# Optimization experiments

Hardware: AMD Instinct MI355X
Metric: run time of the kernel (lower is better)

## Reference

```python
import jax, jax.numpy as jnp
import numpy as np

N = 100000          # nodes
E = 1600000         # edges (nnz of A)
D_IN = 128
D_OUT = 128


def setup_inputs() -> dict:
    key = jax.random.key(0)
    ks = jax.random.split(key, 9)
    s = 1.0 / np.sqrt(D_IN)
    inp = {
        "h_n": jax.random.normal(ks[0], (N, D_IN), dtype=jnp.float32),
        "W_w": jax.random.uniform(ks[1], (D_OUT, D_IN), jnp.float32, -s, s),
        "W_b": jax.random.uniform(ks[2], (D_OUT,), jnp.float32, -s, s),
        "Wt_w": jax.random.uniform(ks[3], (D_OUT, D_IN), jnp.float32, -s, s),
        "Wt_b": jax.random.uniform(ks[4], (D_OUT,), jnp.float32, -s, s),
        "Ws_w": jax.random.uniform(ks[5], (D_OUT, D_IN), jnp.float32, -s, s),
        "Ws_b": jax.random.uniform(ks[6], (D_OUT,), jnp.float32, -s, s),
        # COO indices of sparse adjacency A (binary values): A[rows[e], cols[e]] = 1
        "rows": jax.random.randint(ks[7], (E,), 0, N, dtype=jnp.int64)
                if jax.config.jax_enable_x64 else
                jax.random.randint(ks[7], (E,), 0, N, dtype=jnp.int32),
        "cols": jax.random.randint(ks[8], (E,), 0, N, dtype=jnp.int32),
    }
    inp["rows"] = inp["rows"].astype(jnp.int32)
    return inp


def reference(h_n, W_w, W_b, Wt_w, Wt_b, Ws_w, Ws_b, rows, cols):
    # Dense projections: [N, D_OUT]
    Wh  = h_n @ W_w.T + W_b    # W(h_n)
    Wth = h_n @ Wt_w.T + Wt_b  # W_trans(h_n)
    Wsh = h_n @ Ws_w.T + Ws_b  # W_self(h_n)

    # A @ Wh  : out[i] = sum over edges (i=rows[e], j=cols[e]) of Wh[j]
    agg   = jax.ops.segment_sum(Wh[cols],  rows, num_segments=N)
    # A_T @ Wth : out[i] = sum over edges (j=rows[e], i=cols[e]) of Wth[j]
    agg_t = jax.ops.segment_sum(Wth[rows], cols, num_segments=N)

    # exact (erf-based) GELU, matching torch F.gelu default
    return jax.nn.gelu(agg + agg_t + Wsh, approximate=False)
```

## Files before the change

### kernel.cpp

```cpp
#include <hip/hip_runtime.h>


typedef __bf16 bf16;
typedef __bf16 bf16x4 __attribute__((ext_vector_type(4)));
typedef __bf16 bf16x8 __attribute__((ext_vector_type(8)));
typedef float  f32x4  __attribute__((ext_vector_type(4)));
typedef unsigned int u32;
typedef u32 u32x4 __attribute__((ext_vector_type(4)));
typedef unsigned short u16;

#define D 128
#define CAPC 2432
#define SLAB 2816
#define BIN_CHUNK 6400
#define EPT 25

__global__ __launch_bounds__(256) void k_bin(
    const int* __restrict__ rows, const int* __restrict__ cols,
    int* __restrict__ gcnt_f, int* __restrict__ gcnt_r,
    u32* __restrict__ buf_f, u32* __restrict__ buf_r, int E, int B,
    const float* __restrict__ h,
    const float* __restrict__ Ws_w, const float* __restrict__ W_w,
    const float* __restrict__ Wt_w,
    bf16* __restrict__ h_bf, bf16* __restrict__ wbf, int n4h) {
    __shared__ int hist[1024];
    __shared__ int lbase[1024];
    __shared__ int gbase[1024];
    __shared__ int tsum[256];
    __shared__ u32 sorted[BIN_CHUNK];
    __shared__ u16 btag[BIN_CHUNK];
    int t = threadIdx.x;

    if (blockIdx.y == 2) {
        int stride = gridDim.x * 256;
        int ncast = n4h + 32 + 12288;
        for (int i = blockIdx.x * 256 + t; i < ncast; i += stride) {
            if (i < n4h) {
                f32x4 v = *(const f32x4*)&h[i * 4];
                bf16x4 o;
                o.x = (bf16)v.x; o.y = (bf16)v.y; o.z = (bf16)v.z; o.w = (bf16)v.w;
                *(bf16x4*)&h_bf[i * 4] = o;
            } else if (i < n4h + 32) {
                int k = i - n4h;
                bf16x4 z; z.x = (bf16)0.f; z.y = (bf16)0.f; z.z = (bf16)0.f; z.w = (bf16)0.f;
                *(bf16x4*)&h_bf[(size_t)n4h * 4 + k * 4] = z;
            } else {
                int k = i - n4h - 32;
                const float* src = (k < 4096) ? Ws_w : (k < 8192) ? W_w : Wt_w;
                int kk = k & 4095;
                f32x4 v = *(const f32x4*)&src[kk * 4];
                bf16x4 o;
                o.x = (bf16)v.x; o.y = (bf16)v.y; o.z = (bf16)v.z; o.w = (bf16)v.w;
                *(bf16x4*)&wbf[k * 4] = o;
            }
        }
        return;
    }

    int dir = blockIdx.y;
    const int* key = dir ? cols : rows;
    const int* pay = dir ? rows : cols;
    int* gcnt = dir ? gcnt_r : gcnt_f;
    u32* buf  = dir ? buf_r : buf_f;
    int base = blockIdx.x * BIN_CHUNK;

    for (int b = t; b < 1024; b += 256) hist[b] = 0;
    __syncthreads();
    int kv[EPT], pv[EPT];
#pragma unroll
    for (int i = 0; i < EPT; ++i) {
        int e = base + i * 256 + t;
        if (e < E) {
            kv[i] = key[e]; pv[i] = pay[e];
            atomicAdd(&hist[kv[i] >> 7], 1);
        }
    }
    __syncthreads();
    int s0 = hist[t * 4], s1 = hist[t * 4 + 1], s2 = hist[t * 4 + 2], s3 = hist[t * 4 + 3];
    tsum[t] = s0 + s1 + s2 + s3;
    __syncthreads();
    for (int o = 1; o < 256; o <<= 1) {
        int v = (t >= o) ? tsum[t - o] : 0;
        __syncthreads();
        tsum[t] += v;
        __syncthreads();
    }
    int run = (t > 0) ? tsum[t - 1] : 0;
    lbase[t * 4]     = run;
    lbase[t * 4 + 1] = run + s0;
    lbase[t * 4 + 2] = run + s0 + s1;
    lbase[t * 4 + 3] = run + s0 + s1 + s2;
    __syncthreads();
    int total = tsum[255];
    for (int b = t; b < 1024; b += 256) {
        int nxt = (b < 1023) ? lbase[b + 1] : total;
        int c = nxt - lbase[b];
        gbase[b] = (c && b < B) ? atomicAdd(&gcnt[b], c) : 0;
        hist[b] = lbase[b];
    }
    __syncthreads();
#pragma unroll
    for (int i = 0; i < EPT; ++i) {
        int e = base + i * 256 + t;
        if (e < E) {
            int k = kv[i], p = pv[i];
            int b = k >> 7;
            int pos = atomicAdd(&hist[b], 1);
            sorted[pos] = ((u32)(k & 127) << 17) | (u32)p;
            btag[pos] = (u16)b;
        }
    }
    __syncthreads();
    for (int i = t; i < total; i += 256) {
        int b = btag[i];
        int gp = gbase[b] + (i - lbase[b]);
        if (gp < CAPC) buf[(size_t)b * SLAB + gp] = sorted[i];
    }
}

__device__ __forceinline__ float blo(u32 w) { return __uint_as_float(w << 16); }
__device__ __forceinline__ float bhi(u32 w) { return __uint_as_float(w & 0xffff0000u); }

__global__ __launch_bounds__(256) void k_aggsort(
    const u32* __restrict__ h32,
    const int* __restrict__ gcnt_f, const int* __restrict__ gcnt_r,
    const u32* __restrict__ buf_f, const u32* __restrict__ buf_r,
    bf16* __restrict__ AH, bf16* __restrict__ ATH,
    int* __restrict__ deg_f, int* __restrict__ deg_r, int N, u32 PADV) {
    __shared__ u32 sorted[SLAB];
    __shared__ int hist[128], pscn[128], cursor[128];
    int t = threadIdx.x, bkt = blockIdx.x;
    const int* cp; const u32* buf; bf16* dst; int* deg;
    if (blockIdx.y == 0) { cp = gcnt_f; buf = buf_f + (size_t)bkt * SLAB; dst = AH;  deg = deg_f; }
    else                 { cp = gcnt_r; buf = buf_r + (size_t)bkt * SLAB; dst = ATH; deg = deg_r; }
    int cnt = cp[bkt]; if (cnt > CAPC) cnt = CAPC;
    if (t < 128) hist[t] = 0;
    __syncthreads();
    for (int i = t; i < cnt; i += 256)
        atomicAdd(&hist[buf[i] >> 17], 1);
    __syncthreads();
    int pd = 0;
    if (t < 128) { pd = (hist[t] + 3) & ~3; pscn[t] = pd; }
    __syncthreads();
    for (int o = 1; o < 128; o <<= 1) {
        int v = (t < 128 && t >= o) ? pscn[t - o] : 0;
        __syncthreads();
        if (t < 128) pscn[t] += v;
        __syncthreads();
    }
    int ptot = pscn[127];
    if (t < 128) cursor[t] = pscn[t] - pd;
    __syncthreads();
    for (int i = t; i < ptot; i += 256) sorted[i] = PADV;
    __syncthreads();
    for (int i = t; i < cnt; i += 256) {
        u32 w = buf[i];
        int p = atomicAdd(&cursor[w >> 17], 1);
        sorted[p] = (w & 0x1FFFF) << 6;
    }
    __syncthreads();

    int wave = t >> 6, lane = t & 63;
    int q = lane >> 4, c = lane & 15;
    int node0 = bkt * 128;
    for (int ln = wave; ln < 128; ln += 4) {
        int node = node0 + ln;
        if (node >= N) continue;
        int dg = hist[ln];
        int plen = (dg + 3) & ~3;
        int p = pscn[ln] - plen, pend = pscn[ln];
        float a0 = 0.f, a1 = 0.f, a2 = 0.f, a3 = 0.f;
        float a4 = 0.f, a5 = 0.f, a6 = 0.f, a7 = 0.f;
        for (; p + 15 < pend; p += 16) {
            u32 j0 = sorted[p + q],     j1 = sorted[p + 4 + q];
            u32 j2 = sorted[p + 8 + q], j3 = sorted[p + 12 + q];
            u32x4 w0 = *(const u32x4*)&h32[(size_t)j0 + c * 4];
            u32x4 w1 = *(const u32x4*)&h32[(size_t)j1 + c * 4];
            u32x4 w2 = *(const u32x4*)&h32[(size_t)j2 + c * 4];
            u32x4 w3 = *(const u32x4*)&h32[(size_t)j3 + c * 4];
            a0 += blo(w0.x); a1 += bhi(w0.x); a2 += blo(w0.y); a3 += bhi(w0.y);
            a4 += blo(w0.z); a5 += bhi(w0.z); a6 += blo(w0.w); a7 += bhi(w0.w);
            a0 += blo(w1.x); a1 += bhi(w1.x); a2 += blo(w1.y); a3 += bhi(w1.y);
            a4 += blo(w1.z); a5 += bhi(w1.z); a6 += blo(w1.w); a7 += bhi(w1.w);
            a0 += blo(w2.x); a1 += bhi(w2.x); a2 += blo(w2.y); a3 += bhi(w2.y);
            a4 += blo(w2.z); a5 += bhi(w2.z); a6 += blo(w2.w); a7 += bhi(w2.w);
            a0 += blo(w3.x); a1 += bhi(w3.x); a2 += blo(w3.y); a3 += bhi(w3.y);
            a4 += blo(w3.z); a5 += bhi(w3.z); a6 += blo(w3.w); a7 += bhi(w3.w);
        }
        for (; p + 3 < pend; p += 4) {
            u32 j = sorted[p + q];
            u32x4 w = *(const u32x4*)&h32[(size_t)j + c * 4];
            a0 += blo(w.x); a1 += bhi(w.x); a2 += blo(w.y); a3 += bhi(w.y);
            a4 += blo(w.z); a5 += bhi(w.z); a6 += blo(w.w); a7 += bhi(w.w);
        }
        a0 += __shfl_down(a0, 16); a1 += __shfl_down(a1, 16);
        a2 += __shfl_down(a2, 16); a3 += __shfl_down(a3, 16);
        a4 += __shfl_down(a4, 16); a5 += __shfl_down(a5, 16);
        a6 += __shfl_down(a6, 16); a7 += __shfl_down(a7, 16);
        a0 += __shfl_down(a0, 32); a1 += __shfl_down(a1, 32);
        a2 += __shfl_down(a2, 32); a3 += __shfl_down(a3, 32);
        a4 += __shfl_down(a4, 32); a5 += __shfl_down(a5, 32);
        a6 += __shfl_down(a6, 32); a7 += __shfl_down(a7, 32);
        if (lane < 16) {
            bf16x8 o;
            o[0] = (bf16)a0; o[1] = (bf16)a1; o[2] = (bf16)a2; o[3] = (bf16)a3;
            o[4] = (bf16)a4; o[5] = (bf16)a5; o[6] = (bf16)a6; o[7] = (bf16)a7;
            *(bf16x8*)&dst[(size_t)node * D + c * 8] = o;
        }
    }
    if (t < 128) {
        int node = node0 + t;
        if (node < N) deg[node] = hist[t];
    }
}

__global__ __launch_bounds__(256) void k_gemm(
    const bf16* __restrict__ h, const bf16* __restrict__ AH, const bf16* __restrict__ ATH,
    const bf16* __restrict__ wbf,
    const float* __restrict__ Ws_b, const float* __restrict__ W_b, const float* __restrict__ Wt_b,
    const int* __restrict__ deg_out, const int* __restrict__ deg_in,
    float* __restrict__ out, int N) {
    __shared__ __align__(16) bf16 Ash[128 * 32];
    __shared__ __align__(16) bf16 Bsh[128 * 32];
    int t = threadIdx.x;
    int lane = t & 63;
    int w = t >> 6;
    int wm = (w >> 1) * 64, wn = (w & 1) * 64;
    int m0 = blockIdx.x * 128;

    f32x4 acc[4][4];
#pragma unroll
    for (int i = 0; i < 4; ++i)
#pragma unroll
        for (int j = 0; j < 4; ++j)
            acc[i][j] = (f32x4){0.f, 0.f, 0.f, 0.f};

    for (int kc = 0; kc < 12; ++kc) {
        const bf16* X  = (kc < 4) ? h : (kc < 8) ? AH : ATH;
        const bf16* Wm = wbf + (kc >> 2) * (128 * 128);
        int c0 = (kc & 3) * 32;
#pragma unroll
        for (int r = 0; r < 2; ++r) {
            int v = r * 256 + t;
            int row = v >> 2, seg = v & 3;
            int xr = m0 + row; if (xr >= N) xr = N - 1;
            *(bf16x8*)&Ash[row * 32 + seg * 8] =
                *(const bf16x8*)&X[(size_t)xr * D + c0 + seg * 8];
            *(bf16x8*)&Bsh[row * 32 + seg * 8] =
                *(const bf16x8*)&Wm[row * D + c0 + seg * 8];
        }
        __syncthreads();
        int kg = lane >> 4, lr = lane & 15;
        bf16x8 a[4], b[4];
#pragma unroll
        for (int i = 0; i < 4; ++i) {
            a[i] = *(const bf16x8*)&Ash[(wm + i * 16 + lr) * 32 + kg * 8];
            b[i] = *(const bf16x8*)&Bsh[(wn + i * 16 + lr) * 32 + kg * 8];
        }
#pragma unroll
        for (int i = 0; i < 4; ++i)
#pragma unroll
            for (int j = 0; j < 4; ++j)
                acc[i][j] = __builtin_amdgcn_mfma_f32_16x16x32_bf16(
                    a[i], b[j], acc[i][j], 0, 0, 0);
        __syncthreads();
    }

    int lr = lane & 15, lq = lane >> 4;
#pragma unroll
    for (int i = 0; i < 4; ++i) {
#pragma unroll
        for (int r = 0; r < 4; ++r) {
            int node = m0 + wm + i * 16 + lq * 4 + r;
            if (node >= N) continue;
            float fdr = (float)deg_out[node], fdc = (float)deg_in[node];
#pragma unroll
            for (int j = 0; j < 4; ++j) {
                int f = wn + j * 16 + lr;
                float val = acc[i][j][r] + Ws_b[f] + fdr * W_b[f] + fdc * Wt_b[f];
                float g = 0.5f * val * (1.0f + erff(val * 0.70710678118654752f));
                out[(size_t)node * D + f] = g;
            }
        }
    }
}

extern "C" void kernel_launch(void* const* d_in, const int* in_sizes, int n_in,
                              void* d_out, int out_size, void* d_ws, size_t ws_size,
                              hipStream_t stream) {
    const float* h    = (const float*)d_in[0];
    const float* W_w  = (const float*)d_in[1];
    const float* W_b  = (const float*)d_in[2];
    const float* Wt_w = (const float*)d_in[3];
    const float* Wt_b = (const float*)d_in[4];
    const float* Ws_w = (const float*)d_in[5];
    const float* Ws_b = (const float*)d_in[6];
    const int*   rows = (const int*)d_in[7];
    const int*   cols = (const int*)d_in[8];
    float* out = (float*)d_out;

    const int N = in_sizes[0] / D;
    const int E = in_sizes[7];
    const int B = (N + 127) >> 7;

    char* ws = (char*)d_ws;
    size_t off = 0;
    auto take = [&](size_t bytes) -> char* {
        char* p = ws + off;
        off += (bytes + 511) & ~(size_t)511;
        return p;
    };
    bf16* h_bf    = (bf16*)take((size_t)(N + 1) * D * sizeof(bf16));
    bf16* AH      = (bf16*)take((size_t)N * D * sizeof(bf16));
    bf16* ATH     = (bf16*)take((size_t)N * D * sizeof(bf16));
    bf16* wbf     = (bf16*)take((size_t)3 * 128 * 128 * sizeof(bf16));
    int*  gcnt    = (int*)take((size_t)2 * B * sizeof(int));
    int*  deg_f   = (int*)take((size_t)N * sizeof(int));
    int*  deg_r   = (int*)take((size_t)N * sizeof(int));
    u32*  buf_f   = (u32*)take((size_t)B * SLAB * sizeof(u32));
    u32*  buf_r   = (u32*)take((size_t)B * SLAB * sizeof(u32));
    int*  gcnt_f = gcnt, *gcnt_r = gcnt + B;

    hipMemsetAsync(gcnt, 0, (size_t)2 * B * sizeof(int), stream);

    int n4h = N * D / 4;
    dim3 gbin((E + BIN_CHUNK - 1) / BIN_CHUNK, 3);
    k_bin<<<gbin, 256, 0, stream>>>(rows, cols, gcnt_f, gcnt_r, buf_f, buf_r,
                                    E, B, h, Ws_w, W_w, Wt_w, h_bf, wbf, n4h);
    dim3 gagg(B, 2);
    k_aggsort<<<gagg, 256, 0, stream>>>((const u32*)h_bf, gcnt_f, gcnt_r,
                                        buf_f, buf_r, AH, ATH,
                                        deg_f, deg_r, N, (u32)N << 6);
    k_gemm<<<B, 256, 0, stream>>>(h_bf, AH, ATH, wbf,
                                  Ws_b, W_b, Wt_b,
                                  deg_f, deg_r, out, N);
}
```

Before: 319.7 us.

## Scatter binned edges directly to global slabs, dropping LDS local sort

The binning kernel no longer sorts each chunk's edges in shared memory before writing them out. It now reserves global slab ranges per bucket straight from the histogram, then writes each edge directly using a shared atomic cursor. The per-block chunk is halved, which frees a large amount of LDS and should raise occupancy while removing a scan and a copy pass. The cost is that global writes become scattered instead of contiguous per bucket, which may hurt write coalescing, and more blocks issue global atomics.

```diff
diff --git a/kernel.cpp b/kernel.cpp
--- a/kernel.cpp
+++ b/kernel.cpp
@@ -7,13 +7,12 @@
 typedef float  f32x4  __attribute__((ext_vector_type(4)));
 typedef unsigned int u32;
 typedef u32 u32x4 __attribute__((ext_vector_type(4)));
-typedef unsigned short u16;
 
 #define D 128
 #define CAPC 2432
 #define SLAB 2816
-#define BIN_CHUNK 6400
-#define EPT 25
+#define BIN_CHUNK 3072
+#define EPT 12
 
 __global__ __launch_bounds__(256) void k_bin(
     const int* __restrict__ rows, const int* __restrict__ cols,
@@ -24,11 +23,6 @@
     const float* __restrict__ Wt_w,
     bf16* __restrict__ h_bf, bf16* __restrict__ wbf, int n4h) {
     __shared__ int hist[1024];
-    __shared__ int lbase[1024];
-    __shared__ int gbase[1024];
-    __shared__ int tsum[256];
-    __shared__ u32 sorted[BIN_CHUNK];
-    __shared__ u16 btag[BIN_CHUNK];
     int t = threadIdx.x;
 
     if (blockIdx.y == 2) {
@@ -76,27 +70,9 @@
         }
     }
     __syncthreads();
-    int s0 = hist[t * 4], s1 = hist[t * 4 + 1], s2 = hist[t * 4 + 2], s3 = hist[t * 4 + 3];
-    tsum[t] = s0 + s1 + s2 + s3;
-    __syncthreads();
-    for (int o = 1; o < 256; o <<= 1) {
-        int v = (t >= o) ? tsum[t - o] : 0;
-        __syncthreads();
-        tsum[t] += v;
-        __syncthreads();
-    }
-    int run = (t > 0) ? tsum[t - 1] : 0;
-    lbase[t * 4]     = run;
-    lbase[t * 4 + 1] = run + s0;
-    lbase[t * 4 + 2] = run + s0 + s1;
-    lbase[t * 4 + 3] = run + s0 + s1 + s2;
-    __syncthreads();
-    int total = tsum[255];
     for (int b = t; b < 1024; b += 256) {
-        int nxt = (b < 1023) ? lbase[b + 1] : total;
-        int c = nxt - lbase[b];
-        gbase[b] = (c && b < B) ? atomicAdd(&gcnt[b], c) : 0;
-        hist[b] = lbase[b];
+        int c = hist[b];
+        hist[b] = (c && b < B) ? atomicAdd(&gcnt[b], c) : 0;
     }
     __syncthreads();
 #pragma unroll
@@ -106,15 +82,9 @@
             int k = kv[i], p = pv[i];
             int b = k >> 7;
             int pos = atomicAdd(&hist[b], 1);
-            sorted[pos] = ((u32)(k & 127) << 17) | (u32)p;
-            btag[pos] = (u16)b;
-        }
-    }
-    __syncthreads();
-    for (int i = t; i < total; i += 256) {
-        int b = btag[i];
-        int gp = gbase[b] + (i - lbase[b]);
-        if (gp < CAPC) buf[(size_t)b * SLAB + gp] = sorted[i];
+            if (pos < CAPC)
+                buf[(size_t)b * SLAB + pos] = ((u32)(k & 127) << 17) | (u32)p;
+        }
     }
 }
 
```

New measurement: 327.5 us. +2.4%, slower.

## Fuse neighbor aggregation into GEMM kernel, keeping aggregated tiles in LDS

Applied to the files above, without the earlier changes.

Merges the sort/aggregate kernel and the GEMM kernel into one. Each block handles half of a 128-node bucket, aggregates forward and reverse neighbors into an LDS tile, and immediately multiplies that tile by the corresponding weight matrix. This removes the global AH/ATH and degree round trips and one launch. In exchange, each block re-reads the whole bucket slab and filters it by half, weights are read straight from global memory, and the per-half sort buffer is capped at 1536 entries, so very high-degree halves could be truncated.

```diff
diff --git a/kernel.cpp b/kernel.cpp
--- a/kernel.cpp
+++ b/kernel.cpp
@@ -2,7 +2,7 @@
 
 
 typedef __bf16 bf16;
-typedef __bf16 bf16x4 __attribute__((ext_vector_type(4)));
+typedef __bf16 bf16x4v __attribute__((ext_vector_type(4)));
 typedef __bf16 bf16x8 __attribute__((ext_vector_type(8)));
 typedef float  f32x4  __attribute__((ext_vector_type(4)));
 typedef unsigned int u32;
@@ -11,9 +11,12 @@
 
 #define D 128
 #define CAPC 2432
-#define SLAB 2816
+#define SLAB 2432
 #define BIN_CHUNK 6400
 #define EPT 25
+#define SHALF 1536
+#define TSTR 136
+#define HSTR 40
 
 __global__ __launch_bounds__(256) void k_bin(
     const int* __restrict__ rows, const int* __restrict__ cols,
@@ -37,21 +40,21 @@
         for (int i = blockIdx.x * 256 + t; i < ncast; i += stride) {
             if (i < n4h) {
                 f32x4 v = *(const f32x4*)&h[i * 4];
-                bf16x4 o;
+                bf16x4v o;
                 o.x = (bf16)v.x; o.y = (bf16)v.y; o.z = (bf16)v.z; o.w = (bf16)v.w;
-                *(bf16x4*)&h_bf[i * 4] = o;
+                *(bf16x4v*)&h_bf[i * 4] = o;
             } else if (i < n4h + 32) {
                 int k = i - n4h;
-                bf16x4 z; z.x = (bf16)0.f; z.y = (bf16)0.f; z.z = (bf16)0.f; z.w = (bf16)0.f;
-                *(bf16x4*)&h_bf[(size_t)n4h * 4 + k * 4] = z;
+                bf16x4v z; z.x = (bf16)0.f; z.y = (bf16)0.f; z.z = (bf16)0.f; z.w = (bf16)0.f;
+                *(bf16x4v*)&h_bf[(size_t)n4h * 4 + k * 4] = z;
             } else {
                 int k = i - n4h - 32;
                 const float* src = (k < 4096) ? Ws_w : (k < 8192) ? W_w : Wt_w;
                 int kk = k & 4095;
                 f32x4 v = *(const f32x4*)&src[kk * 4];
-                bf16x4 o;
+                bf16x4v o;
                 o.x = (bf16)v.x; o.y = (bf16)v.y; o.z = (bf16)v.z; o.w = (bf16)v.w;
-                *(bf16x4*)&wbf[k * 4] = o;
+                *(bf16x4v*)&wbf[k * 4] = o;
             }
         }
         return;
@@ -121,144 +124,151 @@
 __device__ __forceinline__ float blo(u32 w) { return __uint_as_float(w << 16); }
 __device__ __forceinline__ float bhi(u32 w) { return __uint_as_float(w & 0xffff0000u); }
 
-__global__ __launch_bounds__(256) void k_aggsort(
-    const u32* __restrict__ h32,
+__global__ __launch_bounds__(256, 6) void k_fused(
+    const u32* __restrict__ h32, const bf16* __restrict__ h_bf,
     const int* __restrict__ gcnt_f, const int* __restrict__ gcnt_r,
     const u32* __restrict__ buf_f, const u32* __restrict__ buf_r,
-    bf16* __restrict__ AH, bf16* __restrict__ ATH,
-    int* __restrict__ deg_f, int* __restrict__ deg_r, int N, u32 PADV) {
-    __shared__ u32 sorted[SLAB];
-    __shared__ int hist[128], pscn[128], cursor[128];
-    int t = threadIdx.x, bkt = blockIdx.x;
-    const int* cp; const u32* buf; bf16* dst; int* deg;
-    if (blockIdx.y == 0) { cp = gcnt_f; buf = buf_f + (size_t)bkt * SLAB; dst = AH;  deg = deg_f; }
-    else                 { cp = gcnt_r; buf = buf_r + (size_t)bkt * SLAB; dst = ATH; deg = deg_r; }
-    int cnt = cp[bkt]; if (cnt > CAPC) cnt = CAPC;
-    if (t < 128) hist[t] = 0;
-    __syncthreads();
-    for (int i = t; i < cnt; i += 256)
-        atomicAdd(&hist[buf[i] >> 17], 1);
-    __syncthreads();
-    int pd = 0;
-    if (t < 128) { pd = (hist[t] + 3) & ~3; pscn[t] = pd; }
-    __syncthreads();
-    for (int o = 1; o < 128; o <<= 1) {
-        int v = (t < 128 && t >= o) ? pscn[t - o] : 0;
-        __syncthreads();
-        if (t < 128) pscn[t] += v;
-        __syncthreads();
-    }
-    int ptot = pscn[127];
-    if (t < 128) cursor[t] = pscn[t] - pd;
-    __syncthreads();
-    for (int i = t; i < ptot; i += 256) sorted[i] = PADV;
-    __syncthreads();
-    for (int i = t; i < cnt; i += 256) {
-        u32 w = buf[i];
-        int p = atomicAdd(&cursor[w >> 17], 1);
-        sorted[p] = (w & 0x1FFFF) << 6;
-    }
-    __syncthreads();
-
-    int wave = t >> 6, lane = t & 63;
-    int q = lane >> 4, c = lane & 15;
-    int node0 = bkt * 128;
-    for (int ln = wave; ln < 128; ln += 4) {
-        int node = node0 + ln;
-        if (node >= N) continue;
-        int dg = hist[ln];
-        int plen = (dg + 3) & ~3;
-        int p = pscn[ln] - plen, pend = pscn[ln];
-        float a0 = 0.f, a1 = 0.f, a2 = 0.f, a3 = 0.f;
-        float a4 = 0.f, a5 = 0.f, a6 = 0.f, a7 = 0.f;
-        for (; p + 15 < pend; p += 16) {
-            u32 j0 = sorted[p + q],     j1 = sorted[p + 4 + q];
-            u32 j2 = sorted[p + 8 + q], j3 = sorted[p + 12 + q];
-            u32x4 w0 = *(const u32x4*)&h32[(size_t)j0 + c * 4];
-            u32x4 w1 = *(const u32x4*)&h32[(size_t)j1 + c * 4];
-            u32x4 w2 = *(const u32x4*)&h32[(size_t)j2 + c * 4];
-            u32x4 w3 = *(const u32x4*)&h32[(size_t)j3 + c * 4];
-            a0 += blo(w0.x); a1 += bhi(w0.x); a2 += blo(w0.y); a3 += bhi(w0.y);
-            a4 += blo(w0.z); a5 += bhi(w0.z); a6 += blo(w0.w); a7 += bhi(w0.w);
-            a0 += blo(w1.x); a1 += bhi(w1.x); a2 += blo(w1.y); a3 += bhi(w1.y);
-            a4 += blo(w1.z); a5 += bhi(w1.z); a6 += blo(w1.w); a7 += bhi(w1.w);
-            a0 += blo(w2.x); a1 += bhi(w2.x); a2 += blo(w2.y); a3 += bhi(w2.y);
-            a4 += blo(w2.z); a5 += bhi(w2.z); a6 += blo(w2.w); a7 += bhi(w2.w);
-            a0 += blo(w3.x); a1 += bhi(w3.x); a2 += blo(w3.y); a3 += bhi(w3.y);
-            a4 += blo(w3.z); a5 += bhi(w3.z); a6 += blo(w3.w); a7 += bhi(w3.w);
-        }
-        for (; p + 3 < pend; p += 4) {
-            u32 j = sorted[p + q];
-            u32x4 w = *(const u32x4*)&h32[(size_t)j + c * 4];
-            a0 += blo(w.x); a1 += bhi(w.x); a2 += blo(w.y); a3 += bhi(w.y);
-            a4 += blo(w.z); a5 += bhi(w.z); a6 += blo(w.w); a7 += bhi(w.w);
-        }
-        a0 += __shfl_down(a0, 16); a1 += __shfl_down(a1, 16);
-        a2 += __shfl_down(a2, 16); a3 += __shfl_down(a3, 16);
-        a4 += __shfl_down(a4, 16); a5 += __shfl_down(a5, 16);
-        a6 += __shfl_down(a6, 16); a7 += __shfl_down(a7, 16);
-        a0 += __shfl_down(a0, 32); a1 += __shfl_down(a1, 32);
-        a2 += __shfl_down(a2, 32); a3 += __shfl_down(a3, 32);
-        a4 += __shfl_down(a4, 32); a5 += __shfl_down(a5, 32);
-        a6 += __shfl_down(a6, 32); a7 += __shfl_down(a7, 32);
-        if (lane < 16) {
-            bf16x8 o;
-            o[0] = (bf16)a0; o[1] = (bf16)a1; o[2] = (bf16)a2; o[3] = (bf16)a3;
-            o[4] = (bf16)a4; o[5] = (bf16)a5; o[6] = (bf16)a6; o[7] = (bf16)a7;
-            *(bf16x8*)&dst[(size_t)node * D + c * 8] = o;
-        }
-    }
-    if (t < 128) {
-        int node = node0 + t;
-        if (node < N) deg[node] = hist[t];
-    }
-}
-
-__global__ __launch_bounds__(256) void k_gemm(
-    const bf16* __restrict__ h, const bf16* __restrict__ AH, const bf16* __restrict__ ATH,
     const bf16* __restrict__ wbf,
-    const float* __restrict__ Ws_b, const float* __restrict__ W_b, const float* __restrict__ Wt_b,
-    const int* __restrict__ deg_out, const int* __restrict__ deg_in,
-    float* __restrict__ out, int N) {
-    __shared__ __align__(16) bf16 Ash[128 * 32];
-    __shared__ __align__(16) bf16 Bsh[128 * 32];
-    int t = threadIdx.x;
-    int lane = t & 63;
-    int w = t >> 6;
-    int wm = (w >> 1) * 64, wn = (w & 1) * 64;
-    int m0 = blockIdx.x * 128;
-
-    f32x4 acc[4][4];
-#pragma unroll
-    for (int i = 0; i < 4; ++i)
+    const float* __restrict__ Ws_b, const float* __restrict__ W_b,
+    const float* __restrict__ Wt_b,
+    float* __restrict__ out, int N, u32 PADV) {
+    __shared__ __align__(16) bf16 Atile[64 * TSTR];
+    __shared__ __align__(16) u32 sortbuf[SHALF];
+    __shared__ int hist[64], pscn[64], cursor[64], degf[64], degr[64];
+    int t = threadIdx.x, lane = t & 63, w = t >> 6;
+    int bkt = blockIdx.x >> 1, half = blockIdx.x & 1;
+    int node0 = bkt * 128 + half * 64;
+    int hbase = half * 64;
+    int lr = lane & 15, kg = lane >> 4;
+    int wm = (w >> 1) * 32, wn = (w & 1) * 64;
+
+    f32x4 acc[2][4];
+#pragma unroll
+    for (int i = 0; i < 2; ++i)
 #pragma unroll
         for (int j = 0; j < 4; ++j)
             acc[i][j] = (f32x4){0.f, 0.f, 0.f, 0.f};
 
-    for (int kc = 0; kc < 12; ++kc) {
-        const bf16* X  = (kc < 4) ? h : (kc < 8) ? AH : ATH;
-        const bf16* Wm = wbf + (kc >> 2) * (128 * 128);
-        int c0 = (kc & 3) * 32;
-#pragma unroll
-        for (int r = 0; r < 2; ++r) {
-            int v = r * 256 + t;
-            int row = v >> 2, seg = v & 3;
-            int xr = m0 + row; if (xr >= N) xr = N - 1;
-            *(bf16x8*)&Ash[row * 32 + seg * 8] =
-                *(const bf16x8*)&X[(size_t)xr * D + c0 + seg * 8];
-            *(bf16x8*)&Bsh[row * 32 + seg * 8] =
-                *(const bf16x8*)&Wm[row * D + c0 + seg * 8];
-        }
-        __syncthreads();
-        int kg = lane >> 4, lr = lane & 15;
-        bf16x8 a[4], b[4];
-#pragma unroll
-        for (int i = 0; i < 4; ++i) {
-            a[i] = *(const bf16x8*)&Ash[(wm + i * 16 + lr) * 32 + kg * 8];
-            b[i] = *(const bf16x8*)&Bsh[(wn + i * 16 + lr) * 32 + kg * 8];
-        }
-#pragma unroll
-        for (int i = 0; i < 4; ++i)
+#pragma unroll 1
+    for (int dir = 0; dir < 2; ++dir) {
+        const u32* buf = (dir ? buf_r : buf_f) + (size_t)bkt * SLAB;
+        int cnt = (dir ? gcnt_r : gcnt_f)[bkt]; if (cnt > CAPC) cnt = CAPC;
+        if (t < 64) hist[t] = 0;
+        __syncthreads();
+        for (int i = t; i < cnt; i += 256) {
+            int ln = (int)(buf[i] >> 17) - hbase;
+            if ((unsigned)ln < 64u) atomicAdd(&hist[ln], 1);
+        }
+        __syncthreads();
+        int pd = 0;
+        if (t < 64) {
+            (dir ? degr : degf)[t] = hist[t];
+            pd = (hist[t] + 3) & ~3; pscn[t] = pd;
+        }
+        __syncthreads();
+        for (int o = 1; o < 64; o <<= 1) {
+            int v = (t < 64 && t >= o) ? pscn[t - o] : 0;
+            __syncthreads();
+            if (t < 64) pscn[t] += v;
+            __syncthreads();
+        }
+        int ptot = pscn[63]; if (ptot > SHALF) ptot = SHALF;
+        if (t < 64) cursor[t] = pscn[t] - pd;
+        __syncthreads();
+        for (int i = t; i < ptot; i += 256) sortbuf[i] = PADV;
+        __syncthreads();
+        for (int i = t; i < cnt; i += 256) {
+            u32 wd = buf[i];
+            int ln = (int)(wd >> 17) - hbase;
+            if ((unsigned)ln < 64u) {
+                int p = atomicAdd(&cursor[ln], 1);
+                if (p < SHALF) sortbuf[p] = (wd & 0x1FFFF) << 6;
+            }
+        }
+        __syncthreads();
+        for (int ln = w; ln < 64; ln += 4) {
+            int plen = (hist[ln] + 3) & ~3;
+            int pend = pscn[ln]; if (pend > SHALF) pend = SHALF;
+            int p = pend - plen; if (p < 0) p = 0;
+            float a0 = 0.f, a1 = 0.f, a2 = 0.f, a3 = 0.f;
+            float a4 = 0.f, a5 = 0.f, a6 = 0.f, a7 = 0.f;
+            for (; p + 15 < pend; p += 16) {
+                u32 j0 = sortbuf[p + kg],     j1 = sortbuf[p + 4 + kg];
+                u32 j2 = sortbuf[p + 8 + kg], j3 = sortbuf[p + 12 + kg];
+                u32x4 w0 = *(const u32x4*)&h32[(size_t)j0 + lr * 4];
+                u32x4 w1 = *(const u32x4*)&h32[(size_t)j1 + lr * 4];
+                u32x4 w2 = *(const u32x4*)&h32[(size_t)j2 + lr * 4];
+                u32x4 w3 = *(const u32x4*)&h32[(size_t)j3 + lr * 4];
+                a0 += blo(w0.x); a1 += bhi(w0.x); a2 += blo(w0.y); a3 += bhi(w0.y);
+                a4 += blo(w0.z); a5 += bhi(w0.z); a6 += blo(w0.w); a7 += bhi(w0.w);
+                a0 += blo(w1.x); a1 += bhi(w1.x); a2 += blo(w1.y); a3 += bhi(w1.y);
+                a4 += blo(w1.z); a5 += bhi(w1.z); a6 += blo(w1.w); a7 += bhi(w1.w);
+                a0 += blo(w2.x); a1 += bhi(w2.x); a2 += blo(w2.y); a3 += bhi(w2.y);
+                a4 += blo(w2.z); a5 += bhi(w2.z); a6 += blo(w2.w); a7 += bhi(w2.w);
+                a0 += blo(w3.x); a1 += bhi(w3.x); a2 += blo(w3.y); a3 += bhi(w3.y);
+                a4 += blo(w3.z); a5 += bhi(w3.z); a6 += blo(w3.w); a7 += bhi(w3.w);
+            }
+            for (; p + 3 < pend; p += 4) {
+                u32 j = sortbuf[p + kg];
+                u32x4 wv = *(const u32x4*)&h32[(size_t)j + lr * 4];
+                a0 += blo(wv.x); a1 += bhi(wv.x); a2 += blo(wv.y); a3 += bhi(wv.y);
+                a4 += blo(wv.z); a5 += bhi(wv.z); a6 += blo(wv.w); a7 += bhi(wv.w);
+            }
+            a0 += __shfl_down(a0, 16); a1 += __shfl_down(a1, 16);
+            a2 += __shfl_down(a2, 16); a3 += __shfl_down(a3, 16);
+            a4 += __shfl_down(a4, 16); a5 += __shfl_down(a5, 16);
+            a6 += __shfl_down(a6, 16); a7 += __shfl_down(a7, 16);
+            a0 += __shfl_down(a0, 32); a1 += __shfl_down(a1, 32);
+            a2 += __shfl_down(a2, 32); a3 += __shfl_down(a3, 32);
+            a4 += __shfl_down(a4, 32); a5 += __shfl_down(a5, 32);
+            a6 += __shfl_down(a6, 32); a7 += __shfl_down(a7, 32);
+            if (lane < 16) {
+                bf16x8 o;
+                o[0] = (bf16)a0; o[1] = (bf16)a1; o[2] = (bf16)a2; o[3] = (bf16)a3;
+                o[4] = (bf16)a4; o[5] = (bf16)a5; o[6] = (bf16)a6; o[7] = (bf16)a7;
+                *(bf16x8*)&Atile[ln * TSTR + lr * 8] = o;
+            }
+        }
+        __syncthreads();
+        const bf16* wmat = wbf + (1 + dir) * (128 * 128);
+#pragma unroll
+        for (int kcl = 0; kcl < 4; ++kcl) {
+            bf16x8 a[2], b[4];
+#pragma unroll
+            for (int i = 0; i < 2; ++i)
+                a[i] = *(const bf16x8*)&Atile[(wm + i * 16 + lr) * TSTR + kcl * 32 + kg * 8];
+#pragma unroll
+            for (int j = 0; j < 4; ++j)
+                b[j] = *(const bf16x8*)&wmat[(size_t)(wn + j * 16 + lr) * D + kcl * 32 + kg * 8];
+#pragma unroll
+            for (int i = 0; i < 2; ++i)
+#pragma unroll
+                for (int j = 0; j < 4; ++j)
+                    acc[i][j] = __builtin_amdgcn_mfma_f32_16x16x32_bf16(
+                        a[i], b[j], acc[i][j], 0, 0, 0);
+        }
+        __syncthreads();
+    }
+
+    bf16* hsh = (bf16*)sortbuf;
+#pragma unroll 1
+    for (int kcl = 0; kcl < 4; ++kcl) {
+        {
+            int row = t >> 2, seg = t & 3;
+            int xr = node0 + row; if (xr > N) xr = N;
+            *(bf16x8*)&hsh[row * HSTR + seg * 8] =
+                *(const bf16x8*)&h_bf[(size_t)xr * D + kcl * 32 + seg * 8];
+        }
+        __syncthreads();
+        bf16x8 a[2], b[4];
+#pragma unroll
+        for (int i = 0; i < 2; ++i)
+            a[i] = *(const bf16x8*)&hsh[(wm + i * 16 + lr) * HSTR + kg * 8];
+#pragma unroll
+        for (int j = 0; j < 4; ++j)
+            b[j] = *(const bf16x8*)&wbf[(size_t)(wn + j * 16 + lr) * D + kcl * 32 + kg * 8];
+#pragma unroll
+        for (int i = 0; i < 2; ++i)
 #pragma unroll
             for (int j = 0; j < 4; ++j)
                 acc[i][j] = __builtin_amdgcn_mfma_f32_16x16x32_bf16(
@@ -266,14 +276,14 @@
         __syncthreads();
     }
 
-    int lr = lane & 15, lq = lane >> 4;
-#pragma unroll
-    for (int i = 0; i < 4; ++i) {
+#pragma unroll
+    for (int i = 0; i < 2; ++i) {
 #pragma unroll
         for (int r = 0; r < 4; ++r) {
-            int node = m0 + wm + i * 16 + lq * 4 + r;
+            int m = wm + i * 16 + kg * 4 + r;
+            int node = node0 + m;
             if (node >= N) continue;
-            float fdr = (float)deg_out[node], fdc = (float)deg_in[node];
+            float fdr = (float)degf[m], fdc = (float)degr[m];
 #pragma unroll
             for (int j = 0; j < 4; ++j) {
                 int f = wn + j * 16 + lr;
@@ -311,12 +321,8 @@
         return p;
     };
     bf16* h_bf    = (bf16*)take((size_t)(N + 1) * D * sizeof(bf16));
-    bf16* AH      = (bf16*)take((size_t)N * D * sizeof(bf16));
-    bf16* ATH     = (bf16*)take((size_t)N * D * sizeof(bf16));
     bf16* wbf     = (bf16*)take((size_t)3 * 128 * 128 * sizeof(bf16));
     int*  gcnt    = (int*)take((size_t)2 * B * sizeof(int));
-    int*  deg_f   = (int*)take((size_t)N * sizeof(int));
-    int*  deg_r   = (int*)take((size_t)N * sizeof(int));
     u32*  buf_f   = (u32*)take((size_t)B * SLAB * sizeof(u32));
     u32*  buf_r   = (u32*)take((size_t)B * SLAB * sizeof(u32));
     int*  gcnt_f = gcnt, *gcnt_r = gcnt + B;
@@ -327,11 +333,8 @@
     dim3 gbin((E + BIN_CHUNK - 1) / BIN_CHUNK, 3);
     k_bin<<<gbin, 256, 0, stream>>>(rows, cols, gcnt_f, gcnt_r, buf_f, buf_r,
                                     E, B, h, Ws_w, W_w, Wt_w, h_bf, wbf, n4h);
-    dim3 gagg(B, 2);
-    k_aggsort<<<gagg, 256, 0, stream>>>((const u32*)h_bf, gcnt_f, gcnt_r,
-                                        buf_f, buf_r, AH, ATH,
-                                        deg_f, deg_r, N, (u32)N << 6);
-    k_gemm<<<B, 256, 0, stream>>>(h_bf, AH, ATH, wbf,
-                                  Ws_b, W_b, Wt_b,
-                                  deg_f, deg_r, out, N);
+    k_fused<<<2 * B, 256, 0, stream>>>((const u32*)h_bf, h_bf, gcnt_f, gcnt_r,
+                                       buf_f, buf_r, wbf,
+                                       Ws_b, W_b, Wt_b,
+                                       out, N, (u32)N << 6);
 }
```

Result: slower. 376.6 us (+17.8%).
